# Optimization experiments

Measured on AMD Instinct MI355X. Metric: run time of the kernel, lower is better.

Reference implementation:

```python
import jax, jax.numpy as jnp
import numpy as np

NEURON_CDECAY = 0.5
NEURON_VDECAY = 0.75
NEURON_VTH = 0.5
PSEUDO_WINDOW = 0.5

@jax.custom_vjp
def pseudo_spike(v):
    return (v > NEURON_VTH).astype(v.dtype)

def _ps_fwd(v):
    return pseudo_spike(v), v

def _ps_bwd(v, g):
    return (g * (jnp.abs(v - NEURON_VTH) < PSEUDO_WINDOW).astype(g.dtype),)

pseudo_spike.defvjp(_ps_fwd, _ps_bwd)

def clif_scan(X_tbd):
    # X_tbd: [T, B, D] synaptic inputs; CLIF neuron recurrence over time.
    def step(carry, x_t):
        c, v, s = carry
        c = c * NEURON_CDECAY + x_t
        v = v * NEURON_VDECAY * (1.0 - s) + c
        s = pseudo_spike(v)
        return (c, v, s), s
    z = jnp.zeros(X_tbd.shape[1:], X_tbd.dtype)
    _, spikes = jax.lax.scan(step, (z, z, z), X_tbd)
    return spikes  # [T, B, D]

def setup_inputs() -> dict:
    key = jax.random.key(0)
    ks = jax.random.split(key, 8)
    B, IN, H1, H2, OUT, T = 256, 2048, 2048, 2048, 1024, 16
    def lin(k, fan_in, fan_out):
        bound = 1.0 / np.sqrt(fan_in)
        kw, kb = jax.random.split(k)
        W = jax.random.uniform(kw, (fan_out, fan_in), jnp.float32, -bound, bound)
        b = jax.random.uniform(kb, (fan_out,), jnp.float32, -bound, bound)
        return W, b
    W0, b0 = lin(ks[0], IN, H1)
    W1, b1 = lin(ks[1], H1, H2)
    W_out, b_out = lin(ks[2], H2, OUT)
    in_pop_spikes = (jax.random.uniform(ks[3], (B, IN, T), jnp.float32) < 0.5).astype(jnp.float32)
    return {"in_pop_spikes": in_pop_spikes, "W0": W0, "b0": b0, "W1": W1, "b1": b1,
            "W_out": W_out, "b_out": b_out, "batch_size": B, "update": 0, "re_calibration": 0}

def reference(in_pop_spikes, W0, b0, W1, b1, W_out, b_out, batch_size, update, re_calibration):
    # layer 0: linear over all timesteps, then CLIF scan
    x = jnp.moveaxis(in_pop_spikes, -1, 0)                    # [T, B, IN]
    s0 = clif_scan(jnp.einsum('tbi,hi->tbh', x, W0) + b0)     # [T, B, H1]
    s1 = clif_scan(jnp.einsum('tbh,gh->tbg', s0, W1) + b1)    # [T, B, H2]
    so = clif_scan(jnp.einsum('tbg,og->tbo', s1, W_out) + b_out)  # [T, B, OUT]
    return jnp.mean(so, axis=0)  # out_pop_act: sum over T / spike_ts
```

## Files before the change

kernel.cpp:

```cpp
#include <hip/hip_runtime.h>
#include <stdint.h>


typedef int v4i __attribute__((ext_vector_type(4)));
typedef int v16i __attribute__((ext_vector_type(16)));

#define TT 16
constexpr int KD = 2048;
constexpr double SCALE = 68719476736.0;

#define GLOAD_LDS16(g, s)                                                      \
  __builtin_amdgcn_global_load_lds(                                            \
      (const __attribute__((address_space(1))) uint32_t*)(g),                  \
      (__attribute__((address_space(3))) uint32_t*)(s), 16, 0, 0)

__device__ __forceinline__ size_t af_addr(int m, int k) {
  return ((size_t)((m >> 5) * 64 + (k >> 5)) << 10)
       + ((size_t)((m & 31) + (((k >> 4) & 1) << 5)) << 4) + (k & 15);
}

__global__ __launch_bounds__(256)
void prep_limbs_all(const float* __restrict__ W0, const float* __restrict__ W1,
                    const float* __restrict__ Wo, int8_t* __restrict__ F0,
                    int8_t* __restrict__ F1, int8_t* __restrict__ Fo) {
  int blk = blockIdx.x;
  const float* W;
  int8_t* dst;
  int total;
  if (blk < 1024)      { W = W0; dst = F0; total = 2048 * 2048; }
  else if (blk < 2048) { W = W1; dst = F1; total = 2048 * 2048; blk -= 1024; }
  else                 { W = Wo; dst = Fo; total = 1024 * 2048; blk -= 2048; }
  const int g = blk * 256 + threadIdx.x;
  const int lane = g & 63;
  const int n = ((g >> 12) << 5) + (lane & 31);
  const int k0 = (((g & 4095) >> 6) << 5) + ((lane >> 5) << 4);
  const float* src = W + (size_t)n * 2048 + k0;
  float4 wv[4];
#pragma unroll
  for (int q = 0; q < 4; ++q) wv[q] = *reinterpret_cast<const float4*>(src + q * 4);
  const float* f = reinterpret_cast<const float*>(wv);
  long long nn[16];
#pragma unroll
  for (int e = 0; e < 16; ++e) nn[e] = (long long)rint((double)f[e] * SCALE);
  const size_t base = (size_t)g * 16;
#pragma unroll
  for (int l = 0; l < 4; ++l) {
    alignas(16) char c[16];
#pragma unroll
    for (int e = 0; e < 16; ++e) {
      const int d = (int)((nn[e] + 128) & 255) - 128;
      c[e] = (char)d;
      nn[e] = (nn[e] - d) >> 8;
    }
    *reinterpret_cast<v4i*>(dst + (size_t)l * total + base) = *(const v4i*)c;
  }
}

__global__ __launch_bounds__(256)
void transpose_x_af(const float* __restrict__ in, int8_t* __restrict__ out) {
  const int idx = blockIdx.x * 256 + threadIdx.x;
  const float4* src = reinterpret_cast<const float4*>(in) + (size_t)idx * 4;
  float4 v[4];
  v[0] = src[0]; v[1] = src[1]; v[2] = src[2]; v[3] = src[3];
  const float* f = reinterpret_cast<const float*>(v);
  const int b = idx >> 11, i = idx & 2047;
  const size_t base = af_addr(b * TT, i);
#pragma unroll
  for (int t = 0; t < TT; ++t) out[base + (size_t)t * 16] = (int8_t)f[t];
}

static __device__ __forceinline__ v16i zero16() {
  v16i z;
#pragma unroll
  for (int i = 0; i < 16; ++i) z[i] = 0;
  return z;
}

template<int N, bool FINAL>
__global__ __launch_bounds__(256, 2)
void gemm_scan_i8(const int8_t* __restrict__ AF,
                  const int8_t* __restrict__ WF,
                  const float* __restrict__ bias,
                  void* __restrict__ outp) {
  __shared__ union SM {
    int8_t buf[3][24 * 1024];
    double c[4][32 * 33];
  } sm;

  const int tid = threadIdx.x;
  const int lane = tid & 63;
  const int w = tid >> 6;
  const int wy = w >> 1, nsub = w & 1;

  constexpr int NN = N / 64;
  constexpr int NWG = 32 * NN;
  const int h = blockIdx.x;
  const int wk = (h & 7) * (NWG >> 3) + (h >> 3);
  const int panel = wk >> 6;
  const int within = wk & 63;
  const int mt = (panel & 3) * 8 + (within & 7);
  const int nt = (panel >> 2) * 8 + (within >> 3);
  const int m0 = mt * 128;
  const int n0 = nt * 64;
  const size_t lst = (size_t)N * KD;

  const int8_t* asrc[2];
  int adst[2];
#pragma unroll
  for (int j = 0; j < 2; ++j) {
    const int fa = w + 4 * j;
    asrc[j] = AF + ((size_t)(((m0 >> 5) + (fa >> 1)) * 64 + (fa & 1)) << 10)
            + lane * 16;
    adst[j] = fa * 1024;
  }
  const int8_t* bsrc[4];
  int bdst[4];
#pragma unroll
  for (int j = 0; j < 4; ++j) {
    const int f = w + 4 * j;
    const int l = f >> 2, kk = (f >> 1) & 1, ns = f & 1;
    bsrc[j] = WF + (size_t)l * lst
            + ((size_t)(((n0 >> 5) + ns) * 64 + kk) << 10) + lane * 16;
    bdst[j] = (8 + f) * 1024;
  }

  v16i acc[4][2];
#pragma unroll
  for (int l = 0; l < 4; ++l) { acc[l][0] = zero16(); acc[l][1] = zero16(); }

  constexpr int NT2 = KD / 64;

#pragma unroll
  for (int j = 0; j < 2; ++j) GLOAD_LDS16(asrc[j], &sm.buf[0][adst[j]]);
#pragma unroll
  for (int j = 0; j < 4; ++j) GLOAD_LDS16(bsrc[j], &sm.buf[0][bdst[j]]);
#pragma unroll
  for (int j = 0; j < 2; ++j) GLOAD_LDS16(asrc[j] + 2048, &sm.buf[1][adst[j]]);
#pragma unroll
  for (int j = 0; j < 4; ++j) GLOAD_LDS16(bsrc[j] + 2048, &sm.buf[1][bdst[j]]);

#define GATE()                                                                 \
  __builtin_amdgcn_s_barrier();                                                \
  asm volatile("s_waitcnt lgkmcnt(0)" ::: "memory");                           \
  __builtin_amdgcn_sched_barrier(0)

#define MFMA4(L, BF)                                                           \
  __builtin_amdgcn_s_setprio(1);                                               \
  acc[L][0] = __builtin_amdgcn_mfma_i32_32x32x32_i8(afr[0][0], BF[0], acc[L][0], 0, 0, 0); \
  acc[L][1] = __builtin_amdgcn_mfma_i32_32x32x32_i8(afr[1][0], BF[0], acc[L][1], 0, 0, 0); \
  acc[L][0] = __builtin_amdgcn_mfma_i32_32x32x32_i8(afr[0][1], BF[1], acc[L][0], 0, 0, 0); \
  acc[L][1] = __builtin_amdgcn_mfma_i32_32x32x32_i8(afr[1][1], BF[1], acc[L][1], 0, 0, 0); \
  __builtin_amdgcn_s_setprio(0)

#define BREAD(BF, L)                                                           \
  BF[0] = *(const v4i*)(bb + ((8 + (((L) << 2) | nsub)) << 10) + lane * 16);   \
  BF[1] = *(const v4i*)(bb + ((8 + (((L) << 2) | 2 | nsub)) << 10) + lane * 16)

  int bufc = 0;
  for (int t2 = 0; t2 < NT2; ++t2) {
    if (t2 == NT2 - 1) asm volatile("s_waitcnt vmcnt(0)" ::: "memory");
    else               asm volatile("s_waitcnt vmcnt(6)" ::: "memory");
    __builtin_amdgcn_s_barrier();
    const int8_t* bb = sm.buf[bufc];
    int b2 = bufc + 2; if (b2 >= 3) b2 -= 3;
    const bool stage = (t2 + 2 < NT2);
    const size_t soff = (size_t)(t2 + 2) * 2048;

    v4i afr[2][2], bf0[2], bf1[2];
    if (stage) {
      GLOAD_LDS16(asrc[0] + soff, &sm.buf[b2][adst[0]]);
      GLOAD_LDS16(asrc[1] + soff, &sm.buf[b2][adst[1]]);
    }
#pragma unroll
    for (int mi = 0; mi < 2; ++mi)
#pragma unroll
      for (int kk = 0; kk < 2; ++kk)
        afr[mi][kk] = *(const v4i*)(bb + ((((wy * 2 + mi) << 1) | kk) << 10)
                                       + lane * 16);
    BREAD(bf0, 0);
    GATE();
    MFMA4(0, bf0);

    if (stage) {
      GLOAD_LDS16(bsrc[0] + soff, &sm.buf[b2][bdst[0]]);
      GLOAD_LDS16(bsrc[1] + soff, &sm.buf[b2][bdst[1]]);
    }
    BREAD(bf1, 1);
    GATE();
    MFMA4(1, bf1);

    if (stage) {
      GLOAD_LDS16(bsrc[2] + soff, &sm.buf[b2][bdst[2]]);
      GLOAD_LDS16(bsrc[3] + soff, &sm.buf[b2][bdst[3]]);
    }
    BREAD(bf0, 2);
    GATE();
    MFMA4(2, bf0);

    BREAD(bf1, 3);
    GATE();
    MFMA4(3, bf1);

    ++bufc; if (bufc == 3) bufc = 0;
  }
#undef BREAD
#undef MFMA4
#undef GATE

  const int rep = (lane & 31) * 0x01010101;
  v4i rowv; rowv[0] = rep; rowv[1] = rep; rowv[2] = rep; rowv[3] = rep;
  v4i onev; onev[0] = 0x01010101; onev[1] = 0x01010101;
            onev[2] = 0x01010101; onev[3] = 0x01010101;
  const v16i drow = __builtin_amdgcn_mfma_i32_32x32x32_i8(rowv, onev, zero16(), 0, 0, 0);
  const v16i dcol = __builtin_amdgcn_mfma_i32_32x32x32_i8(onev, rowv, zero16(), 0, 0, 0);

  const int col = lane & 31;
  const int bl = lane >> 5;
  double* cw = sm.c[w];
#pragma unroll
  for (int mi = 0; mi < 2; ++mi) {
    __syncthreads();
#pragma unroll
    for (int i = 0; i < 16; ++i) {
      long long ts = acc[3][mi][i];
      ts = (ts << 8) + acc[2][mi][i];
      ts = (ts << 8) + acc[1][mi][i];
      ts = (ts << 8) + acc[0][mi][i];
      cw[(drow[i] >> 5) * 33 + (dcol[i] >> 5)] = (double)ts * 0x1p-36;
    }
    __syncthreads();

    const int gn = n0 + nsub * 32 + col;
    const int gm = m0 + (wy * 2 + mi) * 32 + bl * 16;
    const double bj = (double)bias[gn];
    double cc = 0.0, vv = 0.0, ss = 0.0;
    if (!FINAL) {
      int8_t* so = (int8_t*)outp;
      const size_t ab = af_addr(gm, gn);
#pragma unroll
      for (int t = 0; t < TT; ++t) {
        const double x = cw[(bl * 16 + t) * 33 + col] + bj;
        cc = cc * 0.5 + x;
        vv = vv * 0.75 * (1.0 - ss) + cc;
        ss = (vv > 0.5) ? 1.0 : 0.0;
        so[ab + (size_t)t * 16] = (int8_t)ss;
      }
    } else {
      float tot = 0.0f;
#pragma unroll
      for (int t = 0; t < TT; ++t) {
        const double x = cw[(bl * 16 + t) * 33 + col] + bj;
        cc = cc * 0.5 + x;
        vv = vv * 0.75 * (1.0 - ss) + cc;
        ss = (vv > 0.5) ? 1.0 : 0.0;
        tot += (float)ss;
      }
      ((float*)outp)[(size_t)(gm / TT) * N + gn] = tot * 0.0625f;
    }
  }
}

extern "C" void kernel_launch(void* const* d_in, const int* in_sizes, int n_in,
                              void* d_out, int out_size, void* d_ws, size_t ws_size,
                              hipStream_t stream) {
  const float* X  = (const float*)d_in[0];
  const float* W0 = (const float*)d_in[1];
  const float* b0 = (const float*)d_in[2];
  const float* W1 = (const float*)d_in[3];
  const float* b1 = (const float*)d_in[4];
  const float* Wo = (const float*)d_in[5];
  const float* bo = (const float*)d_in[6];
  float* out = (float*)d_out;

  int8_t* base = (int8_t*)d_ws;
  int8_t* AF0 = base;
  int8_t* AF1 = base + (size_t)8388608;
  int8_t* AF2 = AF0;
  int8_t* F0  = base + (size_t)16777216;
  int8_t* F1  = base + (size_t)33554432;
  int8_t* Fo  = base + (size_t)50331648;

  prep_limbs_all<<<2560, 256, 0, stream>>>(W0, W1, Wo, F0, F1, Fo);
  transpose_x_af<<<2048, 256, 0, stream>>>(X, AF0);

  gemm_scan_i8<2048, false><<<1024, 256, 0, stream>>>(AF0, F0, b0, AF1);
  gemm_scan_i8<2048, false><<<1024, 256, 0, stream>>>(AF1, F1, b1, AF2);
  gemm_scan_i8<1024, true ><<< 512, 256, 0, stream>>>(AF2, Fo, bo, out);
}
```

Measured before the change: 186.4 us.

## Drop one int8 weight limb and recompute near-threshold neurons in a fixup pass

Weights are now split into three 8-bit limbs at a 2^28 scale instead of four at 2^36, which removes a quarter of the MFMA work and weight traffic in each GEMM+scan kernel. To keep spike decisions exact, any neuron whose membrane voltage lands within a small band of the threshold is recorded in a flag list through an atomic counter. A new fixup kernel then recomputes those entries with a double-precision dot product against the original fp32 weights. This adds three small kernel launches plus atomics, and the list is capped, so an overflow would leave some entries unrecomputed.

```diff
diff --git a/kernel.cpp b/kernel.cpp
--- a/kernel.cpp
+++ b/kernel.cpp
@@ -7,7 +7,9 @@
 
 #define TT 16
 constexpr int KD = 2048;
-constexpr double SCALE = 68719476736.0;
+constexpr double SCALE = 268435456.0;
+constexpr double BAND = 3.5e-5;
+constexpr uint32_t FCAP = 65536;
 
 #define GLOAD_LDS16(g, s)                                                      \
   __builtin_amdgcn_global_load_lds(                                            \
@@ -44,7 +46,7 @@
   for (int e = 0; e < 16; ++e) nn[e] = (long long)rint((double)f[e] * SCALE);
   const size_t base = (size_t)g * 16;
 #pragma unroll
-  for (int l = 0; l < 4; ++l) {
+  for (int l = 0; l < 3; ++l) {
     alignas(16) char c[16];
 #pragma unroll
     for (int e = 0; e < 16; ++e) {
@@ -69,6 +71,10 @@
   for (int t = 0; t < TT; ++t) out[base + (size_t)t * 16] = (int8_t)f[t];
 }
 
+__global__ void zero_flags(uint32_t* f0, uint32_t* f1, uint32_t* f2) {
+  if (threadIdx.x == 0 && blockIdx.x == 0) { f0[0] = 0; f1[0] = 0; f2[0] = 0; }
+}
+
 static __device__ __forceinline__ v16i zero16() {
   v16i z;
 #pragma unroll
@@ -81,9 +87,10 @@
 void gemm_scan_i8(const int8_t* __restrict__ AF,
                   const int8_t* __restrict__ WF,
                   const float* __restrict__ bias,
-                  void* __restrict__ outp) {
+                  void* __restrict__ outp,
+                  uint32_t* __restrict__ fb) {
   __shared__ union SM {
-    int8_t buf[3][24 * 1024];
+    int8_t buf[3][20 * 1024];
     double c[4][32 * 33];
   } sm;
 
@@ -113,10 +120,10 @@
             + lane * 16;
     adst[j] = fa * 1024;
   }
-  const int8_t* bsrc[4];
-  int bdst[4];
-#pragma unroll
-  for (int j = 0; j < 4; ++j) {
+  const int8_t* bsrc[3];
+  int bdst[3];
+#pragma unroll
+  for (int j = 0; j < 3; ++j) {
     const int f = w + 4 * j;
     const int l = f >> 2, kk = (f >> 1) & 1, ns = f & 1;
     bsrc[j] = WF + (size_t)l * lst
@@ -124,20 +131,20 @@
     bdst[j] = (8 + f) * 1024;
   }
 
-  v16i acc[4][2];
-#pragma unroll
-  for (int l = 0; l < 4; ++l) { acc[l][0] = zero16(); acc[l][1] = zero16(); }
+  v16i acc[3][2];
+#pragma unroll
+  for (int l = 0; l < 3; ++l) { acc[l][0] = zero16(); acc[l][1] = zero16(); }
 
   constexpr int NT2 = KD / 64;
 
 #pragma unroll
   for (int j = 0; j < 2; ++j) GLOAD_LDS16(asrc[j], &sm.buf[0][adst[j]]);
 #pragma unroll
-  for (int j = 0; j < 4; ++j) GLOAD_LDS16(bsrc[j], &sm.buf[0][bdst[j]]);
+  for (int j = 0; j < 3; ++j) GLOAD_LDS16(bsrc[j], &sm.buf[0][bdst[j]]);
 #pragma unroll
   for (int j = 0; j < 2; ++j) GLOAD_LDS16(asrc[j] + 2048, &sm.buf[1][adst[j]]);
 #pragma unroll
-  for (int j = 0; j < 4; ++j) GLOAD_LDS16(bsrc[j] + 2048, &sm.buf[1][bdst[j]]);
+  for (int j = 0; j < 3; ++j) GLOAD_LDS16(bsrc[j] + 2048, &sm.buf[1][bdst[j]]);
 
 #define GATE()                                                                 \
   __builtin_amdgcn_s_barrier();                                                \
@@ -159,7 +166,7 @@
   int bufc = 0;
   for (int t2 = 0; t2 < NT2; ++t2) {
     if (t2 == NT2 - 1) asm volatile("s_waitcnt vmcnt(0)" ::: "memory");
-    else               asm volatile("s_waitcnt vmcnt(6)" ::: "memory");
+    else               asm volatile("s_waitcnt vmcnt(5)" ::: "memory");
     __builtin_amdgcn_s_barrier();
     const int8_t* bb = sm.buf[bufc];
     int b2 = bufc + 2; if (b2 >= 3) b2 -= 3;
@@ -191,15 +198,10 @@
 
     if (stage) {
       GLOAD_LDS16(bsrc[2] + soff, &sm.buf[b2][bdst[2]]);
-      GLOAD_LDS16(bsrc[3] + soff, &sm.buf[b2][bdst[3]]);
     }
     BREAD(bf0, 2);
     GATE();
     MFMA4(2, bf0);
-
-    BREAD(bf1, 3);
-    GATE();
-    MFMA4(3, bf1);
 
     ++bufc; if (bufc == 3) bufc = 0;
   }
@@ -222,11 +224,10 @@
     __syncthreads();
 #pragma unroll
     for (int i = 0; i < 16; ++i) {
-      long long ts = acc[3][mi][i];
-      ts = (ts << 8) + acc[2][mi][i];
+      long long ts = acc[2][mi][i];
       ts = (ts << 8) + acc[1][mi][i];
       ts = (ts << 8) + acc[0][mi][i];
-      cw[(drow[i] >> 5) * 33 + (dcol[i] >> 5)] = (double)ts * 0x1p-36;
+      cw[(drow[i] >> 5) * 33 + (dcol[i] >> 5)] = (double)ts * 0x1p-28;
     }
     __syncthreads();
 
@@ -234,6 +235,7 @@
     const int gm = m0 + (wy * 2 + mi) * 32 + bl * 16;
     const double bj = (double)bias[gn];
     double cc = 0.0, vv = 0.0, ss = 0.0;
+    int flg = 0;
     if (!FINAL) {
       int8_t* so = (int8_t*)outp;
       const size_t ab = af_addr(gm, gn);
@@ -243,6 +245,7 @@
         cc = cc * 0.5 + x;
         vv = vv * 0.75 * (1.0 - ss) + cc;
         ss = (vv > 0.5) ? 1.0 : 0.0;
+        flg |= (fabs(vv - 0.5) < BAND);
         so[ab + (size_t)t * 16] = (int8_t)ss;
       }
     } else {
@@ -253,9 +256,78 @@
         cc = cc * 0.5 + x;
         vv = vv * 0.75 * (1.0 - ss) + cc;
         ss = (vv > 0.5) ? 1.0 : 0.0;
+        flg |= (fabs(vv - 0.5) < BAND);
         tot += (float)ss;
       }
       ((float*)outp)[(size_t)(gm / TT) * N + gn] = tot * 0.0625f;
+    }
+    if (flg) {
+      const uint32_t idx = atomicAdd(&fb[0], 1u);
+      if (idx < FCAP)
+        fb[16 + idx] = ((uint32_t)(gm >> 4) << 11) | (uint32_t)gn;
+    }
+  }
+}
+
+template<int N, bool FINAL>
+__global__ __launch_bounds__(256)
+void fixup(const int8_t* __restrict__ AFin, const float* __restrict__ W,
+           const float* __restrict__ bias, void* __restrict__ outp,
+           const uint32_t* __restrict__ fb) {
+  const int lane = threadIdx.x & 63;
+  const int wv = (blockIdx.x << 2) + (threadIdx.x >> 6);
+  const int nw = gridDim.x << 2;
+  const uint32_t cnt = fb[0] < FCAP ? fb[0] : FCAP;
+  for (uint32_t e = wv; e < cnt; e += nw) {
+    const uint32_t ent = fb[16 + e];
+    const int b = (int)(ent >> 11), n = (int)(ent & 2047);
+    float wr[32];
+#pragma unroll
+    for (int j = 0; j < 32; ++j) wr[j] = W[(size_t)n * KD + lane + 64 * j];
+    double dot[TT];
+#pragma unroll
+    for (int t = 0; t < TT; ++t) dot[t] = 0.0;
+    const int mtile = b >> 1;
+    const int mb = (b & 1) * 16;
+    const int l45 = (lane >> 4) & 1;
+    for (int j = 0; j < 32; ++j) {
+      const size_t ro = ((size_t)(mtile * 64 + 2 * j + (lane >> 5)) << 10)
+                      + (lane & 15);
+#pragma unroll
+      for (int t = 0; t < TT; ++t) {
+        if (AFin[ro + (size_t)(mb + t + 32 * l45) * 16])
+          dot[t] += (double)wr[j];
+      }
+    }
+#pragma unroll
+    for (int t = 0; t < TT; ++t) {
+#pragma unroll
+      for (int off = 32; off >= 1; off >>= 1)
+        dot[t] += __shfl_xor(dot[t], off);
+    }
+    if (lane == 0) {
+      const double bj = (double)bias[n];
+      double cc = 0.0, vv = 0.0, ss = 0.0;
+      if (!FINAL) {
+        int8_t* so = (int8_t*)outp;
+#pragma unroll
+        for (int t = 0; t < TT; ++t) {
+          cc = cc * 0.5 + (dot[t] + bj);
+          vv = vv * 0.75 * (1.0 - ss) + cc;
+          ss = (vv > 0.5) ? 1.0 : 0.0;
+          so[af_addr(TT * b + t, n)] = (int8_t)ss;
+        }
+      } else {
+        float tot = 0.0f;
+#pragma unroll
+        for (int t = 0; t < TT; ++t) {
+          cc = cc * 0.5 + (dot[t] + bj);
+          vv = vv * 0.75 * (1.0 - ss) + cc;
+          ss = (vv > 0.5) ? 1.0 : 0.0;
+          tot += (float)ss;
+        }
+        ((float*)outp)[(size_t)b * N + n] = tot * 0.0625f;
+      }
     }
   }
 }
@@ -277,13 +349,20 @@
   int8_t* AF1 = base + (size_t)8388608;
   int8_t* AF2 = AF0;
   int8_t* F0  = base + (size_t)16777216;
-  int8_t* F1  = base + (size_t)33554432;
-  int8_t* Fo  = base + (size_t)50331648;
-
+  int8_t* F1  = base + (size_t)29360128;
+  int8_t* Fo  = base + (size_t)41943040;
+  uint32_t* FL0 = (uint32_t*)(base + (size_t)48234496);
+  uint32_t* FL1 = (uint32_t*)(base + (size_t)48758784);
+  uint32_t* FL2 = (uint32_t*)(base + (size_t)49283072);
+
+  zero_flags<<<1, 64, 0, stream>>>(FL0, FL1, FL2);
   prep_limbs_all<<<2560, 256, 0, stream>>>(W0, W1, Wo, F0, F1, Fo);
   transpose_x_af<<<2048, 256, 0, stream>>>(X, AF0);
 
-  gemm_scan_i8<2048, false><<<1024, 256, 0, stream>>>(AF0, F0, b0, AF1);
-  gemm_scan_i8<2048, false><<<1024, 256, 0, stream>>>(AF1, F1, b1, AF2);
-  gemm_scan_i8<1024, true ><<< 512, 256, 0, stream>>>(AF2, Fo, bo, out);
-}
+  gemm_scan_i8<2048, false><<<1024, 256, 0, stream>>>(AF0, F0, b0, AF1, FL0);
+  fixup<2048, false><<<128, 256, 0, stream>>>(AF0, W0, b0, AF1, FL0);
+  gemm_scan_i8<2048, false><<<1024, 256, 0, stream>>>(AF1, F1, b1, AF2, FL1);
+  fixup<2048, false><<<128, 256, 0, stream>>>(AF1, W1, b1, AF2, FL1);
+  gemm_scan_i8<1024, true ><<< 512, 256, 0, stream>>>(AF2, Fo, bo, out, FL2);
+  fixup<1024, true ><<<128, 256, 0, stream>>>(AF2, Wo, bo, out, FL2);
+}
```

New measurement: 216.6 us. 16.2% more time.
